# Kernel tuning notes

Hardware: AMD Instinct MI355X
Metric: run time of the kernel (lower is better)

Reference implementation:

```python
import jax, jax.numpy as jnp
import numpy as np

B, S, HID = 1, 2048, 2048
NH, NKV = 16, 4
HD = HID // NH  # 128


def _rope_manual(x, cos_h, sin_h):
    # x: [B, S, nh, HD]; cos_h/sin_h: [1, S, 1, HD//2]
    d = x.shape[-1]
    x_rot = x[..., : d // 2]
    x_pass = x[..., d // 2:]
    # rotate interleaved pairs inside the first half
    x_rot = jnp.stack([-x_rot[..., 1::2], x_rot[..., ::2]], axis=-1)
    x_rot = x_rot.reshape(x_rot.shape[:-2] + (d // 2,))
    return jnp.concatenate(
        [x_rot * cos_h + x_pass * sin_h, -x_rot * sin_h + x_pass * cos_h], axis=-1
    )


def setup_inputs() -> dict:
    key = jax.random.key(0)
    ks = jax.random.split(key, 7)
    bound = 1.0 / np.sqrt(HID)
    return {
        "x": jax.random.normal(ks[0], (B, S, HID), jnp.float32),
        "cos": jax.random.uniform(ks[1], (S, HD), jnp.float32),
        "sin": jax.random.uniform(ks[2], (S, HD), jnp.float32),
        "wq": jax.random.uniform(ks[3], (NH * HD, HID), jnp.float32, -bound, bound),
        "wk": jax.random.uniform(ks[4], (NKV * HD, HID), jnp.float32, -bound, bound),
        "wv": jax.random.uniform(ks[5], (NKV * HD, HID), jnp.float32, -bound, bound),
        "wo": jax.random.uniform(ks[6], (HID, HID), jnp.float32, -bound, bound),
    }


def reference(x, cos, sin, wq, wk, wv, wo):
    b, s, _ = x.shape
    q = jnp.einsum("bsh,oh->bso", x, wq).reshape(b, s, NH, HD)
    k = jnp.einsum("bsh,oh->bso", x, wk).reshape(b, s, NKV, HD)
    v = jnp.einsum("bsh,oh->bso", x, wv).reshape(b, s, NKV, HD)

    cos_h = cos[None, :, None, : HD // 2]  # [1,S,1,HD/2]
    sin_h = sin[None, :, None, : HD // 2]
    q = _rope_manual(q, cos_h, sin_h)
    k = _rope_manual(k, cos_h, sin_h)

    # [B, H, S, D]
    q = q.transpose(0, 2, 1, 3)
    k = k.transpose(0, 2, 1, 3)
    v = v.transpose(0, 2, 1, 3)
    # GQA kv repeat (repeat_interleave over head dim)
    rep = NH // NKV
    k = jnp.repeat(k, rep, axis=1)
    v = jnp.repeat(v, rep, axis=1)

    scale = 1.0 / np.sqrt(HD).astype(np.float32)
    scores = jnp.einsum("bhqd,bhkd->bhqk", q, k) * scale
    causal = jnp.tril(jnp.ones((s, s), bool))
    scores = jnp.where(causal[None, None], scores, jnp.finfo(scores.dtype).min)
    attn = jax.nn.softmax(scores, axis=-1)
    out = jnp.einsum("bhqk,bhkd->bhqd", attn, v)  # [B,H,S,D]
    out = out.transpose(0, 2, 1, 3).reshape(b, s, NH * HD)
    return jnp.einsum("bso,ho->bsh", out, wo)
```

## Files before the change

kernel.cpp:

```cpp
#include <hip/hip_runtime.h>
#include <hip/hip_bf16.h>

typedef __bf16 bf16_t;
typedef __attribute__((ext_vector_type(8))) __bf16 bf16x8;
typedef __attribute__((ext_vector_type(4))) __bf16 bf16x4;
typedef __attribute__((ext_vector_type(4))) float f32x4;

#define S_LEN 2048
#define HID 2048
#define NH 16
#define NKV 4
#define HD 128

__device__ __forceinline__ void gll16(const bf16_t* g, bf16_t* l) {
    __builtin_amdgcn_global_load_lds(
        (const __attribute__((address_space(1))) unsigned int*)g,
        (__attribute__((address_space(3))) unsigned int*)l, 16, 0, 0);
}

__device__ __forceinline__ bf16x8 cvt2x4(float4 a, float4 b) {
    bf16x8 o;
    o[0]=(bf16_t)a.x; o[1]=(bf16_t)a.y; o[2]=(bf16_t)a.z; o[3]=(bf16_t)a.w;
    o[4]=(bf16_t)b.x; o[5]=(bf16_t)b.y; o[6]=(bf16_t)b.z; o[7]=(bf16_t)b.w;
    return o;
}

__global__ __launch_bounds__(256) void cvt_f32_bf16(const float* __restrict__ in,
                                                    bf16_t* __restrict__ out, int n)
{
    int i = (blockIdx.x * 256 + threadIdx.x) * 8;
    if (i >= n) return;
    float4 a = *(const float4*)&in[i];
    float4 b = *(const float4*)&in[i + 4];
    *(bf16x8*)&out[i] = cvt2x4(a, b);
}

__global__ __launch_bounds__(256) void cvt_w3(const float* __restrict__ wq,
                                              const float* __restrict__ wk,
                                              const float* __restrict__ wv,
                                              bf16_t* __restrict__ out)
{
    int i = (blockIdx.x * 256 + threadIdx.x) * 8;
    const float* src; int off;
    if (i < 4 * 1024 * 1024)      { src = wq; off = i; }
    else if (i < 5 * 1024 * 1024) { src = wk; off = i - 4 * 1024 * 1024; }
    else                          { src = wv; off = i - 5 * 1024 * 1024; }
    float4 a = *(const float4*)&src[off];
    float4 b = *(const float4*)&src[off + 4];
    *(bf16x8*)&out[i] = cvt2x4(a, b);
}

template<int MODE, typename CT>
__global__ __launch_bounds__(256, 4) void gemm128x64(
    const bf16_t* __restrict__ A, const bf16_t* __restrict__ B,
    CT* __restrict__ C, bf16_t* __restrict__ CkP, bf16_t* __restrict__ CvtP,
    int N, int K)
{
    __shared__ __align__(16) bf16_t sA[128 * 64];
    __shared__ __align__(16) bf16_t sB[64 * 64];

    const int tid = threadIdx.x, lane = tid & 63, wave = tid >> 6;
    const int l16 = lane & 15, quad = lane >> 4;
    const int m0 = blockIdx.y * 128, n0 = blockIdx.x * 64;
    const int wm = (wave >> 1) * 64, wn = (wave & 1) * 32;

    const bf16_t* gA[4]; const bf16_t* gB[2];
    bf16_t* lA[4]; bf16_t* lB[2];
#pragma unroll
    for (int t = 0; t < 4; t++) {
        int p = (wave * 4 + t) * 64 + lane;
        int row = p >> 3;
        int lc = (p & 7) ^ (row & 7);
        gA[t] = A + (size_t)(m0 + row) * K + lc * 8;
        lA[t] = &sA[(wave * 4 + t) * 512];
    }
#pragma unroll
    for (int t = 0; t < 2; t++) {
        int p = (wave * 2 + t) * 64 + lane;
        int row = p >> 3;
        int lc = (p & 7) ^ (row & 7);
        gB[t] = B + (size_t)(n0 + row) * K + lc * 8;
        lB[t] = &sB[(wave * 2 + t) * 512];
    }

    int offA[2][4], offB[2][2];
#pragma unroll
    for (int kc = 0; kc < 2; kc++) {
#pragma unroll
        for (int i = 0; i < 4; i++) {
            int rm = wm + i * 16 + l16;
            offA[kc][i] = rm * 64 + (((kc * 4 + quad) ^ (rm & 7)) * 8);
        }
#pragma unroll
        for (int j = 0; j < 2; j++) {
            int rn = wn + j * 16 + l16;
            offB[kc][j] = rn * 64 + (((kc * 4 + quad) ^ (rn & 7)) * 8);
        }
    }

    f32x4 acc[4][2] = {};

    for (int k0 = 0; k0 < K; k0 += 64) {
        __syncthreads();
#pragma unroll
        for (int t = 0; t < 4; t++) { gll16(gA[t], lA[t]); gA[t] += 64; }
#pragma unroll
        for (int t = 0; t < 2; t++) { gll16(gB[t], lB[t]); gB[t] += 64; }
        __syncthreads();

#pragma unroll
        for (int kc = 0; kc < 2; kc++) {
            bf16x8 af[4], bfv[2];
#pragma unroll
            for (int i = 0; i < 4; i++) af[i] = *(bf16x8*)&sA[offA[kc][i]];
#pragma unroll
            for (int j = 0; j < 2; j++) bfv[j] = *(bf16x8*)&sB[offB[kc][j]];
#pragma unroll
            for (int i = 0; i < 4; i++)
#pragma unroll
                for (int j = 0; j < 2; j++)
                    acc[i][j] = __builtin_amdgcn_mfma_f32_16x16x32_bf16(af[i], bfv[j], acc[i][j], 0, 0, 0);
        }
    }

#pragma unroll
    for (int i = 0; i < 4; i++) {
        int rowb = m0 + wm + i * 16 + quad * 4;
#pragma unroll
        for (int j = 0; j < 2; j++) {
            int col = n0 + wn + j * 16 + l16;
#pragma unroll
            for (int r = 0; r < 4; r++) {
                float v = acc[i][j][r];
                int row = rowb + r;
                if (MODE == 0) {
                    C[(size_t)row * N + col] = (CT)v;
                } else {
                    if (col < 2048)      C[(size_t)row * 2048 + col] = (CT)v;
                    else if (col < 2560) CkP[(size_t)row * 512 + (col - 2048)] = (bf16_t)v;
                    else                 CvtP[(size_t)(col - 2560) * S_LEN + row] = (bf16_t)v;
                }
            }
        }
    }
}

__global__ void rope_all(bf16_t* __restrict__ Qh, bf16_t* __restrict__ Kh,
                         const float* __restrict__ cosb, const float* __restrict__ sinb)
{
    int s = blockIdx.x;
    int grp = blockIdx.y;
    int sub = threadIdx.x >> 5;
    int i = threadIdx.x & 31;
    bf16_t* row = (grp < 4) ? (Qh + ((size_t)s * NH + grp * 4 + sub) * HD)
                            : (Kh + ((size_t)s * NKV + sub) * HD);
    float x0 = (float)row[2 * i];
    float x1 = (float)row[2 * i + 1];
    float p0 = (float)row[64 + 2 * i];
    float p1 = (float)row[64 + 2 * i + 1];
    float c0 = cosb[s * HD + 2 * i];
    float c1 = cosb[s * HD + 2 * i + 1];
    float n0 = sinb[s * HD + 2 * i];
    float n1 = sinb[s * HD + 2 * i + 1];
    float r0 = -x1, r1 = x0;
    row[2 * i]          = (bf16_t)(r0 * c0 + p0 * n0);
    row[2 * i + 1]      = (bf16_t)(r1 * c1 + p1 * n1);
    row[64 + 2 * i]     = (bf16_t)(-r0 * n0 + p0 * c0);
    row[64 + 2 * i + 1] = (bf16_t)(-r1 * n1 + p1 * c1);
}

__global__ __launch_bounds__(512, 1) void flash_attn10(
    const bf16_t* __restrict__ Q,
    const bf16_t* __restrict__ Kb,
    const bf16_t* __restrict__ VT,
    bf16_t* __restrict__ OpD,
    bf16_t* __restrict__ OpX,
    float* __restrict__ lpart,
    int S)
{
    __shared__ __align__(16) bf16_t sK[2][64 * 136];
    __shared__ __align__(16) bf16_t sVT[2][128 * 72];
    __shared__ __align__(16) bf16_t sP[8][16 * 72];

    const int c   = blockIdx.x;
    const int kvh = blockIdx.y;
    const int p   = c >> 2, sub = c & 3;
    const int ts   = (33 * sub + 3) >> 2;
    const int tend = (33 * sub + 36) >> 2;
    const int tA   = p + 1;

    const int tid = threadIdx.x, lane = tid & 63, wave = tid >> 6;
    const int l16 = lane & 15, quad = lane >> 4;
    const int rowg = wave & 3;
    const int h0   = kvh * 4 + (wave >> 2) * 2;
    const float scale = 0.08838834764831845f;

    int krow[2], kcol[2], vrow[2], vcol[2];
#pragma unroll
    for (int it = 0; it < 2; it++) {
        int cc = tid + 512 * it;
        krow[it] = cc >> 4; kcol[it] = (cc & 15) * 8;
        vrow[it] = cc >> 3; vcol[it] = (cc & 7) * 8;
    }

#pragma unroll
    for (int sI = 0; sI < 2; sI++) {
        int st0, st1, sqt, ssl;
        if (sI == 0) {
            if (ts < tA) { st0 = ts; st1 = (tend < tA ? tend : tA); sqt = p;      ssl = c; }
            else         { st0 = ts; st1 = tend;                    sqt = 31 - p; ssl = c; }
        } else {
            if (!(ts < tA && tend > tA)) break;
            st0 = tA; st1 = tend; sqt = 31 - p; ssl = 64 + p;
        }
        const int base = (sqt == p) ? 0 : tA;
        const int kb = st0 - base, ke = st1 - base;
        const int qt = sqt;
        const int q0 = qt * 64;
        const int qrow = q0 + rowg * 16 + l16;

        bf16x8 qf[2][4];
#pragma unroll
        for (int h = 0; h < 2; h++)
#pragma unroll
            for (int cc = 0; cc < 4; cc++)
                qf[h][cc] = *(const bf16x8*)&Q[(size_t)qrow * HID + (h0 + h) * HD + cc * 32 + quad * 8];

        f32x4 oacc[2][8] = {};
        float lsum[2] = {0.f, 0.f};

        bf16x8 kpre[2], vpre[2];
#pragma unroll
        for (int it = 0; it < 2; it++) {
            kpre[it] = *(const bf16x8*)&Kb[(size_t)(kb * 64 + krow[it]) * (NKV * HD) + kvh * HD + kcol[it]];
            vpre[it] = *(const bf16x8*)&VT[((size_t)kvh * HD + vrow[it]) * S + kb * 64 + vcol[it]];
        }
#pragma unroll
        for (int it = 0; it < 2; it++) {
            *(bf16x8*)&sK[0][krow[it] * 136 + kcol[it]] = kpre[it];
            *(bf16x8*)&sVT[0][vrow[it] * 72 + vcol[it]] = vpre[it];
        }
        if (kb + 1 < ke) {
            const int t1 = (kb + 1) * 64;
#pragma unroll
            for (int it = 0; it < 2; it++) {
                kpre[it] = *(const bf16x8*)&Kb[(size_t)(t1 + krow[it]) * (NKV * HD) + kvh * HD + kcol[it]];
                vpre[it] = *(const bf16x8*)&VT[((size_t)kvh * HD + vrow[it]) * S + t1 + vcol[it]];
            }
        }
        __syncthreads();

        int sel = 0;
        for (int kt = kb; kt < ke; kt++) {
            const int t0 = kt * 64;
            const int ns = sel ^ 1;

            if (kt + 1 < ke) {
#pragma unroll
                for (int it = 0; it < 2; it++) {
                    *(bf16x8*)&sK[ns][krow[it] * 136 + kcol[it]] = kpre[it];
                    *(bf16x8*)&sVT[ns][vrow[it] * 72 + vcol[it]] = vpre[it];
                }
                if (kt + 2 < ke) {
                    const int t2 = t0 + 128;
#pragma unroll
                    for (int it = 0; it < 2; it++) {
                        kpre[it] = *(const bf16x8*)&Kb[(size_t)(t2 + krow[it]) * (NKV * HD) + kvh * HD + kcol[it]];
                        vpre[it] = *(const bf16x8*)&VT[((size_t)kvh * HD + vrow[it]) * S + t2 + vcol[it]];
                    }
                }
            }

            f32x4 sc[2][4];
            __builtin_amdgcn_s_setprio(1);
#pragma unroll
            for (int nt = 0; nt < 4; nt++) {
                bf16x8 kf[4];
#pragma unroll
                for (int cc = 0; cc < 4; cc++)
                    kf[cc] = *(bf16x8*)&sK[sel][(nt * 16 + l16) * 136 + cc * 32 + quad * 8];
#pragma unroll
                for (int h = 0; h < 2; h++) {
                    f32x4 d = {};
#pragma unroll
                    for (int cc = 0; cc < 4; cc++)
                        d = __builtin_amdgcn_mfma_f32_16x16x32_bf16(kf[cc], qf[h][cc], d, 0, 0, 0);
                    sc[h][nt] = d;
                }
            }
            __builtin_amdgcn_s_setprio(0);

            bf16x8 pa[2][2];
            if (kt == qt) {
#pragma unroll
                for (int h = 0; h < 2; h++) {
#pragma unroll
                    for (int nt = 0; nt < 4; nt++) {
                        const int tbk = t0 + nt * 16 + quad * 4;
                        bf16x4 pk;
#pragma unroll
                        for (int r = 0; r < 4; r++) {
                            float pv = (tbk + r <= qrow) ? __expf(sc[h][nt][r] * scale) : 0.0f;
                            lsum[h] += pv;
                            pk[r] = (bf16_t)pv;
                        }
                        *(bf16x4*)&sP[wave][l16 * 72 + nt * 16 + quad * 4] = pk;
                    }
#pragma unroll
                    for (int kc = 0; kc < 2; kc++)
                        pa[h][kc] = *(bf16x8*)&sP[wave][l16 * 72 + kc * 32 + quad * 8];
                }
            } else {
#pragma unroll
                for (int h = 0; h < 2; h++) {
#pragma unroll
                    for (int nt = 0; nt < 4; nt++) {
                        bf16x4 pk;
#pragma unroll
                        for (int r = 0; r < 4; r++) {
                            float pv = __expf(sc[h][nt][r] * scale);
                            lsum[h] += pv;
                            pk[r] = (bf16_t)pv;
                        }
                        *(bf16x4*)&sP[wave][l16 * 72 + nt * 16 + quad * 4] = pk;
                    }
#pragma unroll
                    for (int kc = 0; kc < 2; kc++)
                        pa[h][kc] = *(bf16x8*)&sP[wave][l16 * 72 + kc * 32 + quad * 8];
                }
            }

            __builtin_amdgcn_s_setprio(1);
#pragma unroll
            for (int dt = 0; dt < 8; dt++)
#pragma unroll
                for (int kc = 0; kc < 2; kc++) {
                    bf16x8 vf = *(bf16x8*)&sVT[sel][(dt * 16 + l16) * 72 + kc * 32 + quad * 8];
#pragma unroll
                    for (int h = 0; h < 2; h++)
                        oacc[h][dt] = __builtin_amdgcn_mfma_f32_16x16x32_bf16(pa[h][kc], vf, oacc[h][dt], 0, 0, 0);
                }
            __builtin_amdgcn_s_setprio(0);

            __syncthreads();
            sel = ns;
        }

        const int sg = kvh * 80 + ssl;
        bf16_t* Op = (sg < 256) ? (OpD + (size_t)sg * 32768)
                                : (OpX + (size_t)(sg - 256) * 32768);
#pragma unroll
        for (int h = 0; h < 2; h++) {
            const int hl = (wave >> 2) * 2 + h;
            float lr = lsum[h];
            lr += __shfl_xor(lr, 16, 64);
            lr += __shfl_xor(lr, 32, 64);
            if (quad == 0)
                lpart[(size_t)sg * 256 + (rowg * 16 + l16) * 4 + hl] = lr;
#pragma unroll
            for (int r = 0; r < 4; r++) {
                int rr = rowg * 16 + quad * 4 + r;
#pragma unroll
                for (int dt = 0; dt < 8; dt++)
                    Op[((size_t)rr * 4 + hl) * 128 + dt * 16 + l16] =
                        (bf16_t)(oacc[h][dt][r]);
            }
        }
    }
}

__global__ __launch_bounds__(256) void flash_combine10(
    const bf16_t* __restrict__ OpD, const bf16_t* __restrict__ OpX,
    const float* __restrict__ lpart, bf16_t* __restrict__ oh)
{
    int i = (blockIdx.x * 256 + threadIdx.x) * 8;
    int s = i >> 11;
    int h = (i >> 7) & 15;
    int col = i & 127;
    int qt = s >> 6;
    int base80 = (h >> 2) * 80;
    int roff = (s & 63) * 4 + (h & 3);

    int sl[4]; int nsl = 0;
    if (qt <= 15) {
        int pr = qt;
#pragma unroll
        for (int sub = 0; sub < 4; sub++) {
            int tss = (33 * sub + 3) >> 2;
            if (tss < qt + 1) sl[nsl++] = pr * 4 + sub;
        }
    } else {
        int pr = 31 - qt, tAh = pr + 1;
#pragma unroll
        for (int sub = 0; sub < 4; sub++) {
            int tss = (33 * sub + 3) >> 2;
            int ten = (33 * sub + 36) >> 2;
            if (ten > tAh) sl[nsl++] = (tss < tAh) ? 64 + pr : pr * 4 + sub;
        }
    }

    float acc[8] = {0.f, 0.f, 0.f, 0.f, 0.f, 0.f, 0.f, 0.f};
    float l = 0.f;
    for (int ci = 0; ci < nsl; ci++) {
        int sg = base80 + sl[ci];
        const bf16_t* P = (sg < 256) ? (OpD + (size_t)sg * 32768)
                                     : (OpX + (size_t)(sg - 256) * 32768);
        bf16x8 a = *(const bf16x8*)&P[(size_t)roff * 128 + col];
#pragma unroll
        for (int j = 0; j < 8; j++) acc[j] += (float)a[j];
        l += lpart[(size_t)sg * 256 + roff];
    }
    float inv = 1.0f / l;
    bf16x8 o;
#pragma unroll
    for (int j = 0; j < 8; j++)
        o[j] = (bf16_t)(acc[j] * inv);
    *(bf16x8*)&oh[i] = o;
}

extern "C" void kernel_launch(void* const* d_in, const int* in_sizes, int n_in,
                              void* d_out, int out_size, void* d_ws, size_t ws_size,
                              hipStream_t stream)
{
    const float* x    = (const float*)d_in[0];
    const float* cosb = (const float*)d_in[1];
    const float* sinb = (const float*)d_in[2];
    const float* wq   = (const float*)d_in[3];
    const float* wk   = (const float*)d_in[4];
    const float* wv   = (const float*)d_in[5];
    const float* wo   = (const float*)d_in[6];
    float* out = (float*)d_out;

    char* ws = (char*)d_ws;
    bf16_t* wb = (bf16_t*)(ws);
    bf16_t* qh = (bf16_t*)(ws + (size_t)12 * 1024 * 1024);
    bf16_t* kh = (bf16_t*)(ws + (size_t)20 * 1024 * 1024);
    bf16_t* vT = (bf16_t*)(ws + (size_t)22 * 1024 * 1024);
    float*  lp = (float*) (ws + (size_t)24 * 1024 * 1024);
    bf16_t* opx = (bf16_t*)(ws + (size_t)24 * 1024 * 1024 + 512 * 1024);
    bf16_t* xb  = (bf16_t*)d_out;
    bf16_t* opd = (bf16_t*)d_out;

    const int NX = S_LEN * HID;

    cvt_f32_bf16<<<NX / (256 * 8), 256, 0, stream>>>(x, xb, NX);

    cvt_w3<<<6 * 1024 * 1024 / (256 * 8), 256, 0, stream>>>(wq, wk, wv, wb);

    gemm128x64<1, bf16_t><<<dim3(48, 16), 256, 0, stream>>>(xb, wb, qh, kh, vT, 3072, HID);

    rope_all<<<dim3(S_LEN, 5), 128, 0, stream>>>(qh, kh, cosb, sinb);

    flash_attn10<<<dim3(64, NKV), 512, 0, stream>>>(qh, kh, vT, opd, opx, lp, S_LEN);

    flash_combine10<<<NX / (256 * 8), 256, 0, stream>>>(opd, opx, lp, qh);

    cvt_f32_bf16<<<NX / (256 * 8), 256, 0, stream>>>(wo, wb, NX);

    gemm128x64<0, float><<<dim3(32, 16), 256, 0, stream>>>(qh, wb, out, nullptr, nullptr, HID, HID);
}
```

Before: 214.6 us.

## Double-buffer GEMM LDS tiles and merge input conversion kernels

The GEMM now double-buffers its shared-memory tiles. It prefetches the next K-slice with global_load_lds while computing on the current one, so each iteration needs one barrier instead of two. The x and wq/wk/wv conversions are merged into a single launch, and the wo conversion is moved earlier in the stream. This doubles LDS per block (48KB), which may reduce occupancy under the 4-blocks launch bound, and relies on async LDS loads finishing before the barrier.

After: 212.9 us. Within noise of the previous version (-0.8%).

```diff
diff --git a/kernel.cpp b/kernel.cpp
--- a/kernel.cpp
+++ b/kernel.cpp
@@ -25,6 +25,27 @@
     return o;
 }
 
+__global__ __launch_bounds__(256) void cvt_all(
+    const float* __restrict__ x,  const float* __restrict__ wq,
+    const float* __restrict__ wk, const float* __restrict__ wv,
+    bf16_t* __restrict__ xb, bf16_t* __restrict__ wb)
+{
+    const size_t M = 1024 * 1024;
+    size_t g = ((size_t)blockIdx.x * 256 + threadIdx.x) * 8;
+    const float* src; bf16_t* dst; size_t soff, doff;
+    if (g < 4 * M) {
+        src = x; dst = xb; soff = g; doff = g;
+    } else {
+        size_t w = g - 4 * M; dst = wb; doff = w;
+        if (w < 4 * M)      { src = wq; soff = w; }
+        else if (w < 5 * M) { src = wk; soff = w - 4 * M; }
+        else                { src = wv; soff = w - 5 * M; }
+    }
+    float4 a = *(const float4*)&src[soff];
+    float4 b = *(const float4*)&src[soff + 4];
+    *(bf16x8*)&dst[doff] = cvt2x4(a, b);
+}
+
 __global__ __launch_bounds__(256) void cvt_f32_bf16(const float* __restrict__ in,
                                                     bf16_t* __restrict__ out, int n)
 {
@@ -35,29 +56,14 @@
     *(bf16x8*)&out[i] = cvt2x4(a, b);
 }
 
-__global__ __launch_bounds__(256) void cvt_w3(const float* __restrict__ wq,
-                                              const float* __restrict__ wk,
-                                              const float* __restrict__ wv,
-                                              bf16_t* __restrict__ out)
-{
-    int i = (blockIdx.x * 256 + threadIdx.x) * 8;
-    const float* src; int off;
-    if (i < 4 * 1024 * 1024)      { src = wq; off = i; }
-    else if (i < 5 * 1024 * 1024) { src = wk; off = i - 4 * 1024 * 1024; }
-    else                          { src = wv; off = i - 5 * 1024 * 1024; }
-    float4 a = *(const float4*)&src[off];
-    float4 b = *(const float4*)&src[off + 4];
-    *(bf16x8*)&out[i] = cvt2x4(a, b);
-}
-
 template<int MODE, typename CT>
 __global__ __launch_bounds__(256, 4) void gemm128x64(
     const bf16_t* __restrict__ A, const bf16_t* __restrict__ B,
     CT* __restrict__ C, bf16_t* __restrict__ CkP, bf16_t* __restrict__ CvtP,
     int N, int K)
 {
-    __shared__ __align__(16) bf16_t sA[128 * 64];
-    __shared__ __align__(16) bf16_t sB[64 * 64];
+    __shared__ __align__(16) bf16_t sA[2][128 * 64];
+    __shared__ __align__(16) bf16_t sB[2][64 * 64];
 
     const int tid = threadIdx.x, lane = tid & 63, wave = tid >> 6;
     const int l16 = lane & 15, quad = lane >> 4;
@@ -65,14 +71,14 @@
     const int wm = (wave >> 1) * 64, wn = (wave & 1) * 32;
 
     const bf16_t* gA[4]; const bf16_t* gB[2];
-    bf16_t* lA[4]; bf16_t* lB[2];
+    int laOff[4], lbOff[2];
 #pragma unroll
     for (int t = 0; t < 4; t++) {
         int p = (wave * 4 + t) * 64 + lane;
         int row = p >> 3;
         int lc = (p & 7) ^ (row & 7);
         gA[t] = A + (size_t)(m0 + row) * K + lc * 8;
-        lA[t] = &sA[(wave * 4 + t) * 512];
+        laOff[t] = (wave * 4 + t) * 512;
     }
 #pragma unroll
     for (int t = 0; t < 2; t++) {
@@ -80,7 +86,7 @@
         int row = p >> 3;
         int lc = (p & 7) ^ (row & 7);
         gB[t] = B + (size_t)(n0 + row) * K + lc * 8;
-        lB[t] = &sB[(wave * 2 + t) * 512];
+        lbOff[t] = (wave * 2 + t) * 512;
     }
 
     int offA[2][4], offB[2][2];
@@ -100,27 +106,38 @@
 
     f32x4 acc[4][2] = {};
 
+#pragma unroll
+    for (int t = 0; t < 4; t++) { gll16(gA[t], &sA[0][laOff[t]]); gA[t] += 64; }
+#pragma unroll
+    for (int t = 0; t < 2; t++) { gll16(gB[t], &sB[0][lbOff[t]]); gB[t] += 64; }
+    __syncthreads();
+
+    int bsel = 0;
     for (int k0 = 0; k0 < K; k0 += 64) {
-        __syncthreads();
-#pragma unroll
-        for (int t = 0; t < 4; t++) { gll16(gA[t], lA[t]); gA[t] += 64; }
-#pragma unroll
-        for (int t = 0; t < 2; t++) { gll16(gB[t], lB[t]); gB[t] += 64; }
-        __syncthreads();
+        const int ns = bsel ^ 1;
+        if (k0 + 64 < K) {
+#pragma unroll
+            for (int t = 0; t < 4; t++) { gll16(gA[t], &sA[ns][laOff[t]]); gA[t] += 64; }
+#pragma unroll
+            for (int t = 0; t < 2; t++) { gll16(gB[t], &sB[ns][lbOff[t]]); gB[t] += 64; }
+        }
 
 #pragma unroll
         for (int kc = 0; kc < 2; kc++) {
             bf16x8 af[4], bfv[2];
 #pragma unroll
-            for (int i = 0; i < 4; i++) af[i] = *(bf16x8*)&sA[offA[kc][i]];
-#pragma unroll
-            for (int j = 0; j < 2; j++) bfv[j] = *(bf16x8*)&sB[offB[kc][j]];
+            for (int i = 0; i < 4; i++) af[i] = *(bf16x8*)&sA[bsel][offA[kc][i]];
+#pragma unroll
+            for (int j = 0; j < 2; j++) bfv[j] = *(bf16x8*)&sB[bsel][offB[kc][j]];
 #pragma unroll
             for (int i = 0; i < 4; i++)
 #pragma unroll
                 for (int j = 0; j < 2; j++)
                     acc[i][j] = __builtin_amdgcn_mfma_f32_16x16x32_bf16(af[i], bfv[j], acc[i][j], 0, 0, 0);
         }
+
+        __syncthreads();
+        bsel = ns;
     }
 
 #pragma unroll
@@ -443,19 +460,18 @@
 
     const int NX = S_LEN * HID;
 
-    cvt_f32_bf16<<<NX / (256 * 8), 256, 0, stream>>>(x, xb, NX);
-
-    cvt_w3<<<6 * 1024 * 1024 / (256 * 8), 256, 0, stream>>>(wq, wk, wv, wb);
+    cvt_all<<<10 * 1024 * 1024 / (256 * 8), 256, 0, stream>>>(
+        x, wq, wk, wv, xb, wb);
 
     gemm128x64<1, bf16_t><<<dim3(48, 16), 256, 0, stream>>>(xb, wb, qh, kh, vT, 3072, HID);
 
     rope_all<<<dim3(S_LEN, 5), 128, 0, stream>>>(qh, kh, cosb, sinb);
 
+    cvt_f32_bf16<<<NX / (256 * 8), 256, 0, stream>>>(wo, wb, NX);
+
     flash_attn10<<<dim3(64, NKV), 512, 0, stream>>>(qh, kh, vT, opd, opx, lp, S_LEN);
 
     flash_combine10<<<NX / (256 * 8), 256, 0, stream>>>(opd, opx, lp, qh);
 
-    cvt_f32_bf16<<<NX / (256 * 8), 256, 0, stream>>>(wo, wb, NX);
-
     gemm128x64<0, float><<<dim3(32, 16), 256, 0, stream>>>(qh, wb, out, nullptr, nullptr, HID, HID);
 }
```
